# Kernel optimization log

Hardware: AMD Instinct MI355X
Metric: run time of the kernel (lower is better)

The kernel has to match this reference:

```python
import jax, jax.numpy as jnp
import numpy as np

S, V, H = 32, 16, 8            # hidden_scalars, hidden_vectors, num_heads
N, E = 10000, 100000           # nodes, edges
NRB, RH = 16, 64               # radial basis, radial MLP hidden
TH = S + 3 * V                 # packed irreps width (80)
WNUM = S * S + V * S + S * V + 2 * V * V  # TP weight_numel = 2560


def setup_inputs() -> dict:
    key = jax.random.key(0)
    ks = jax.random.split(key, 16)
    inp = {}
    inp["node_features"] = jax.random.normal(ks[0], (N, TH), jnp.float32)
    inp["edge_index"] = jax.random.randint(ks[1], (2, E), 0, N)
    inp["edge_sh"] = jax.random.normal(ks[2], (E, 4), jnp.float32)
    inp["edge_radial"] = jax.random.uniform(ks[3], (E, NRB), dtype=jnp.float32)
    inp["edge_envelope"] = jax.random.uniform(ks[4], (E,), dtype=jnp.float32)
    # radial MLP
    inp["W1"] = jax.random.normal(ks[5], (NRB, RH), jnp.float32) / np.sqrt(NRB)
    inp["b1"] = jnp.zeros((RH,), jnp.float32)
    inp["W2"] = jax.random.normal(ks[6], (RH, WNUM), jnp.float32) / np.sqrt(RH)
    inp["b2"] = jnp.zeros((WNUM,), jnp.float32)
    # attention query/key nets (scalar channels only)
    inp["Wq"] = jax.random.normal(ks[7], (S, H), jnp.float32) / np.sqrt(S)
    inp["bq"] = jnp.zeros((H,), jnp.float32)
    inp["Wk"] = jax.random.normal(ks[8], (S, H), jnp.float32) / np.sqrt(S)
    inp["bk"] = jnp.zeros((H,), jnp.float32)
    # equivariant linears (per-irrep channel mixing, e3nn style, no bias)
    inp["Wout_s"] = jax.random.normal(ks[9], (S, S), jnp.float32)
    inp["Wout_v"] = jax.random.normal(ks[10], (V, V), jnp.float32)
    inp["Wg_s"] = jax.random.normal(ks[11], (S, S + V), jnp.float32)
    inp["Wg_v"] = jax.random.normal(ks[12], (V, V), jnp.float32)
    # equivariant batch norm params
    inp["bn_ws"] = jnp.ones((S,), jnp.float32)
    inp["bn_bs"] = jnp.zeros((S,), jnp.float32)
    inp["bn_wv"] = jnp.ones((V,), jnp.float32)
    return inp


def _forward(node_features, edge_sh, edge_radial, edge_envelope,
             W1, b1, W2, b2, Wq, bq, Wk, bk,
             Wout_s, Wout_v, Wg_s, Wg_v, bn_ws, bn_bs, bn_wv, src, dst):
    # --- per-edge TP weights from radial MLP -> (E, WNUM), the big tensor ---
    tp_w = jax.nn.silu(edge_radial @ W1 + b1) @ W2 + b2
    offs = np.cumsum([0, S * S, V * S, S * V, V * V, V * V])
    WA = tp_w[:, offs[0]:offs[1]].reshape(-1, S, S)  # 0e x 0e -> 0e
    WB = tp_w[:, offs[1]:offs[2]].reshape(-1, V, S)  # 1o x 1o -> 0e
    WC = tp_w[:, offs[2]:offs[3]].reshape(-1, S, V)  # 0e x 1o -> 1o
    WD = tp_w[:, offs[3]:offs[4]].reshape(-1, V, V)  # 1o x 0e -> 1o
    WE = tp_w[:, offs[4]:offs[5]].reshape(-1, V, V)  # 1o x 1o -> 1o (cross)

    # --- gather source features, split irreps ---
    s_src = node_features[src, :S]                       # (E, S)
    v_src = node_features[src, S:].reshape(-1, V, 3)     # (E, V, 3)
    y0 = edge_sh[:, 0:1]                                 # (E, 1) l=0
    y1 = edge_sh[:, 1:4]                                 # (E, 3) l=1

    a0 = 1.0 / np.sqrt(S + V)       # path normalization, 0e output
    a1 = 1.0 / np.sqrt(S + 2 * V)   # path normalization, 1o output

    dot = (v_src * y1[:, None, :]).sum(-1) / np.sqrt(3.0)          # (E, V)
    msg_s = a0 * (jnp.einsum('es,esk->ek', s_src * y0, WA)
                  + jnp.einsum('ev,evk->ek', dot, WB))             # (E, S)
    crs = jnp.cross(v_src, y1[:, None, :]) / np.sqrt(2.0)          # (E, V, 3)
    msg_v = a1 * (jnp.einsum('es,ec,esk->ekc', s_src, y1, WC)
                  + jnp.einsum('evc,evk->ekc', v_src * y0[:, :, None], WD)
                  + jnp.einsum('evc,evk->ekc', crs, WE))           # (E, V, 3)
    messages = jnp.concatenate([msg_s, msg_v.reshape(-1, 3 * V)], axis=-1)

    # --- scatter-softmax attention over incoming edges per destination ---
    q = node_features[dst, :S] @ Wq + bq                 # (E, H)
    k = msg_s @ Wk + bk                                  # (E, H)
    logits = (q * k).sum(-1) / np.sqrt(H) + jnp.log(edge_envelope + 1e-8)
    mx = jax.ops.segment_max(logits, dst, num_segments=N)
    ex = jnp.exp(logits - mx[dst])
    den = jax.ops.segment_sum(ex, dst, num_segments=N)
    attn = ex / (den[dst] + 1e-8)                        # (E,)

    agg = jax.ops.segment_sum(attn[:, None] * messages, dst, num_segments=N)

    # --- equivariant output linear ---
    agg_s = agg[:, :S] @ Wout_s / np.sqrt(S)
    agg_v = jnp.einsum('nvc,vw->nwc', agg[:, S:].reshape(-1, V, 3), Wout_v) / np.sqrt(V)

    # --- gate ---
    gs = agg_s @ Wg_s / np.sqrt(S)                       # (N, S+V)
    gv = jnp.einsum('nvc,vw->nwc', agg_v, Wg_v) / np.sqrt(V)
    s = jax.nn.silu(gs[:, :S])
    g = jax.nn.sigmoid(gs[:, S:])
    v = g[:, :, None] * gv
    act = jnp.concatenate([s, v.reshape(-1, 3 * V)], axis=-1)

    # --- residual + equivariant batch norm ---
    x = act + node_features
    xs = x[:, :S]
    xv = x[:, S:].reshape(-1, V, 3)
    mean = xs.mean(0)
    var = xs.var(0)
    xs = (xs - mean) / jnp.sqrt(var + 1e-5) * bn_ws + bn_bs
    vn = (xv * xv).mean(-1).mean(0)                      # (V,) component norm
    xv = xv * (bn_wv / jnp.sqrt(vn + 1e-5))[None, :, None]
    return jnp.concatenate([xs, xv.reshape(-1, 3 * V)], axis=-1)


def reference(node_features, edge_index, edge_sh, edge_radial, edge_envelope,
              W1, b1, W2, b2, Wq, bq, Wk, bk,
              Wout_s, Wout_v, Wg_s, Wg_v, bn_ws, bn_bs, bn_wv):
    src, dst = edge_index[0], edge_index[1]
    return _forward(node_features, edge_sh, edge_radial, edge_envelope,
                    W1, b1, W2, b2, Wq, bq, Wk, bk,
                    Wout_s, Wout_v, Wg_s, Wg_v, bn_ws, bn_bs, bn_wv, src, dst)
```

## Files before the change

### kernel.cpp

```cpp
#include <hip/hip_runtime.h>
#include <math.h>

typedef __bf16 bf16x8 __attribute__((ext_vector_type(8)));
typedef __bf16 bf16x4 __attribute__((ext_vector_type(4)));
typedef float  f32x4  __attribute__((ext_vector_type(4)));
typedef float  f32x2  __attribute__((ext_vector_type(2)));
typedef unsigned long long u64x2 __attribute__((ext_vector_type(2)));

__device__ __forceinline__ float silu_f(float x){ return x / (1.f + __expf(-x)); }
__device__ __forceinline__ float sigm_f(float x){ return 1.f / (1.f + __expf(-x)); }

__device__ __forceinline__ float ntld_f(const float* p){
  return __builtin_nontemporal_load(p);
}
__device__ __forceinline__ float ntbf(const __bf16* p){
  unsigned short us = __builtin_nontemporal_load((const unsigned short*)p);
  union { unsigned u; float f; } cv; cv.u = ((unsigned)us) << 16;
  return cv.f;
}
__device__ __forceinline__ void nt_store_f(float* p, float v){
  __builtin_nontemporal_store(v, p);
}
__device__ __forceinline__ void nt_store_b8(__bf16* p, bf16x8 v){
  u64x2 u; __builtin_memcpy(&u, &v, 16);
  __builtin_nontemporal_store(u, (u64x2*)p);
}
__device__ __forceinline__ f32x2 b4lo(bf16x4 v){ f32x2 r; r[0]=(float)v[0]; r[1]=(float)v[1]; return r; }
__device__ __forceinline__ f32x2 b4hi(bf16x4 v){ f32x2 r; r[0]=(float)v[2]; r[1]=(float)v[3]; return r; }

__global__ void __launch_bounds__(256) k_setup(const float* __restrict__ W2,
    __bf16* __restrict__ W2t, const int* __restrict__ ei, int* __restrict__ cnt,
    const float* __restrict__ nf, const float* __restrict__ Wq,
    const float* __restrict__ bq, const float* __restrict__ Wk,
    const float* __restrict__ bk, float* __restrict__ kvt, float* __restrict__ carr,
    int nbPrep, int nbHist, int N, int E){
  int b = blockIdx.x, t = threadIdx.x;
  if (b < nbPrep){
    int gid = b*256 + t;
    int h = gid / 2560;
    int col = gid - h*2560;
    W2t[(size_t)(h>>5)*81920 + col*32 + (h&31)] = (__bf16)ntld_f(&W2[gid]);
    return;
  }
  if (b < nbPrep + nbHist){
    int e = (b - nbPrep)*256 + t;
    if (e < E) atomicAdd(&cnt[ei[E+e]], 1);
    return;
  }
  __shared__ float M[32][33];
  __shared__ float mb[32];
  __shared__ float nfl[64][33];
  __shared__ float bqbk_s;
  const int n0 = (b - nbPrep - nbHist)*64;
  for (int idx = t; idx < 1024; idx += 256){
    int s = idx >> 5, i = idx & 31;
    float acc = 0.f;
    #pragma unroll
    for (int j = 0; j < 8; ++j) acc += Wq[s*8+j]*Wk[i*8+j];
    M[s][i] = acc;
  }
  if (t < 32){
    float acc = 0.f;
    #pragma unroll
    for (int j = 0; j < 8; ++j) acc += Wq[t*8+j]*bk[j];
    mb[t] = acc;
  }
  if (t == 0){
    float acc = 0.f;
    #pragma unroll
    for (int j = 0; j < 8; ++j) acc += bq[j]*bk[j];
    bqbk_s = acc;
  }
  for (int idx = t; idx < 2048; idx += 256){
    int nl = idx >> 5, s = idx & 31;
    int n = n0 + nl;
    nfl[nl][s] = (n < N) ? nf[(size_t)n*80 + s] : 0.f;
  }
  __syncthreads();
  for (int idx = t; idx < 2048; idx += 256){
    int nl = idx >> 5, i = idx & 31;
    int n = n0 + nl;
    if (n < N){
      float acc = 0.f;
      #pragma unroll 8
      for (int s = 0; s < 32; ++s) acc += nfl[nl][s]*M[s][i];
      kvt[(size_t)n*32 + i] = acc;
    }
  }
  if (t < 64){
    int n = n0 + t;
    if (n < N){
      float acc = bqbk_s;
      #pragma unroll 8
      for (int s = 0; s < 32; ++s) acc += nfl[t][s]*mb[s];
      carr[n] = acc;
    }
  }
}

__global__ void __launch_bounds__(1024) k_scan(const int* __restrict__ cnt,
    int* __restrict__ cursor, float* __restrict__ bnacc, int N, int E){
  __shared__ int part[1024];
  int t = threadIdx.x;
  if (t < 80) bnacc[t] = 0.f;
  int chunk = (N + 1023) >> 10;
  int lo = t*chunk, hi = min(lo+chunk, N);
  int s = 0;
  for (int i = lo; i < hi; ++i) s += cnt[i];
  part[t] = s;
  __syncthreads();
  for (int off = 1; off < 1024; off <<= 1){
    int v = (t >= off) ? part[t-off] : 0;
    __syncthreads();
    part[t] += v;
    __syncthreads();
  }
  int base = (t == 0) ? 0 : part[t-1];
  for (int i = lo; i < hi; ++i){
    cursor[i] = base;
    base += cnt[i];
  }
}

__global__ void __launch_bounds__(256) k_prep(
    const float* __restrict__ nf, const int* __restrict__ ei,
    const float* __restrict__ sh, const float* __restrict__ radial,
    const float* __restrict__ W1, const float* __restrict__ b1,
    int* __restrict__ cursor,
    __bf16* __restrict__ uG, __bf16* __restrict__ cabG, __bf16* __restrict__ cvG,
    int* __restrict__ permG, int E, int NT)
{
  __shared__ float featT[80][65];
  __shared__ float radl[64][17];
  __shared__ float shlT[4][64];
  __shared__ float w1l[1024];
  __shared__ float b1l[64];
  __shared__ __align__(16) __bf16 u_l[64][72];
  __shared__ __align__(16) __bf16 cab_l[48][64];
  __shared__ __align__(16) __bf16 cv_l[64][3][64];
  __shared__ int src_l[64];

  const int t = threadIdx.x;
  const int e0 = blockIdx.x*64;
  const int tg0 = blockIdx.x*4;

  if (t < 64){
    int ee = e0 + t;
    if (ee < E){
      src_l[t] = ei[ee];
      permG[ee] = atomicAdd(&cursor[ei[(size_t)E+ee]], 1);
    } else src_l[t] = ei[E-1];
    b1l[t] = b1[t];
  }
  {
    int e = t >> 2, c = t & 3;
    int ec = min(e0+e, E-1);
    shlT[c][e] = ntld_f(&sh[(size_t)ec*4+c]);
  }
  for (int i = t; i < 1024; i += 256){
    int e = i >> 4, r = i & 15;
    int ec = min(e0+e, E-1);
    radl[e][r] = ntld_f(&radial[(size_t)ec*16+r]);
  }
  *(float4*)&w1l[t*4] = ((const float4*)W1)[t];
  __syncthreads();

  for (int i = t; i < 5120; i += 256){
    int e = i / 80, idx = i - e*80;
    featT[idx][e] = nf[(size_t)src_l[e]*80 + idx];
  }
  for (int i = t; i < 4096; i += 256){
    int e = i & 63, h = i >> 6;
    float acc = b1l[h];
    #pragma unroll
    for (int r = 0; r < 16; ++r) acc += radl[e][r]*w1l[r*64+h];
    u_l[e][h] = (__bf16)silu_f(acc);
  }
  __syncthreads();

  const float inv_s3 = 0.57735026918962576f;
  const float inv_s2 = 0.70710678118654752f;
  const float a0 = 0.14433756729740643f;
  const float a1 = 0.125f;

  for (int i = t; i < 3072; i += 256){
    int r = i >> 6, e = i & 63;
    float val;
    if (r < 32) val = a0 * shlT[0][e] * featT[r][e];
    else {
      int v = r - 32;
      float dot = (featT[32+v*3][e]*shlT[1][e] + featT[33+v*3][e]*shlT[2][e]
                 + featT[34+v*3][e]*shlT[3][e]) * inv_s3;
      val = a0 * dot;
    }
    cab_l[r][e] = (__bf16)val;
  }
  for (int i = t; i < 12288; i += 256){
    int e = i & 63, r = (i >> 6) & 63, c = i >> 12;
    float val;
    if (r < 32) val = a1 * shlT[1+c][e] * featT[r][e];
    else if (r < 48){
      int v = r - 32;
      val = a1 * shlT[0][e] * featT[32+v*3+c][e];
    } else {
      int v = r - 48;
      int c1 = c+1; if (c1 > 2) c1 -= 3;
      int c2 = c+2; if (c2 > 2) c2 -= 3;
      val = a1 * inv_s2 * (featT[32+v*3+c1][e]*shlT[1+c2][e]
                         - featT[32+v*3+c2][e]*shlT[1+c1][e]);
    }
    cv_l[r][c][e] = (__bf16)val;
  }
  __syncthreads();

  for (int i = t; i < 512; i += 256){
    int tl = i >> 7, rem = i & 127, k8 = rem >> 4, e = rem & 15;
    if (tg0 + tl < NT){
      bf16x8 v = *(const bf16x8*)&u_l[tl*16 + e][k8*8];
      *(bf16x8*)((char*)uG + (size_t)(tg0+tl)*2048 + k8*256 + e*16) = v;
    }
  }
  for (int i = t; i < 384; i += 256){
    int tl = i / 96, rem = i - tl*96, r = rem >> 1, h = rem & 1;
    if (tg0 + tl < NT){
      bf16x8 v = *(const bf16x8*)&cab_l[r][tl*16 + h*8];
      *(bf16x8*)((char*)cabG + (size_t)(tg0+tl)*1536 + r*32 + h*16) = v;
    }
  }
  for (int i = t; i < 1536; i += 256){
    int tl = i / 384, rem = i - tl*384, r = rem / 6, rem2 = rem - r*6,
        c = rem2 >> 1, h = rem2 & 1;
    if (tg0 + tl < NT){
      bf16x8 v = *(const bf16x8*)&cv_l[r][c][tl*16 + h*8];
      *(bf16x8*)((char*)cvG + (size_t)(tg0+tl)*6144 + r*96 + c*32 + h*16) = v;
    }
  }
}

#define LOAD_PANEL(BASE_IT, NITS) do {                                         \
    for (int idx = t; idx < (NITS)*128; idx += 1024){                          \
      int itl_ = idx >> 7, rem_ = idx & 127, half_ = rem_ >> 6, r6_ = rem_ & 63;\
      int col_ = r6_ >> 2, quad_ = r6_ & 3;                                    \
      *(float4*)(panel + itl_*2048 + half_*1024 + quad_*256 + col_*16) =       \
        *(const float4*)(w2b + half_*163840 + (size_t)((BASE_IT)+itl_)*1024    \
                         + col_*64 + quad_*16);                                \
    }                                                                          \
    for (int i = t; i < (NITS)*16; i += 1024) b2l[i] = b2[(BASE_IT)*16 + i];   \
  } while(0)

#define CAB_STAGE(TGC, BASE) do {                                              \
    bf16x8 x_ = *(const bf16x8*)(cabGb + (size_t)(TGC)*1536 + lane*16);        \
    bf16x4 y_ = *(const bf16x4*)(cabGb + (size_t)(TGC)*1536 + 1024 + lane*8);  \
    *(bf16x8*)(myCab + (BASE) + lane*16) = x_;                                 \
    *(bf16x4*)(myCab + (BASE) + 1024 + lane*8) = y_;                           \
  } while(0)

#define CV_STAGE_SUB(TGC, BASE, HALF, SUB) do {                                \
    const char* s_ = cvGb + (size_t)(TGC)*6144 + (HALF)*3072 + (SUB)*1536      \
                   + lane*24;                                                  \
    bf16x4 a_ = *(const bf16x4*)(s_);                                          \
    bf16x4 b_ = *(const bf16x4*)(s_ + 8);                                      \
    bf16x4 c_ = *(const bf16x4*)(s_ + 16);                                     \
    *(bf16x4*)(myCab + (BASE) + lane*24)      = a_;                            \
    *(bf16x4*)(myCab + (BASE) + lane*24 + 8)  = b_;                            \
    *(bf16x4*)(myCab + (BASE) + lane*24 + 16) = c_;                            \
  } while(0)

#define S_PAIR(SECOND, CBA, CBB, TA, TB) do {                                  \
    _Pragma("unroll 4")                                                        \
    for (int itl = 0; itl < 48; ++itl){                                        \
      bf16x8 B0_ = *(const bf16x8*)(panel + itl*2048 + laneOff);               \
      bf16x8 B1_ = *(const bf16x8*)(panel + itl*2048 + 1024 + laneOff);        \
      f32x4 dA_; dA_[0]=0;dA_[1]=0;dA_[2]=0;dA_[3]=0; f32x4 dB_ = dA_;         \
      dA_ = __builtin_amdgcn_mfma_f32_16x16x32_bf16(u##TA##_0, B0_, dA_, 0,0,0);\
      dB_ = __builtin_amdgcn_mfma_f32_16x16x32_bf16(u##TB##_0, B0_, dB_, 0,0,0);\
      dA_ = __builtin_amdgcn_mfma_f32_16x16x32_bf16(u##TA##_1, B1_, dA_, 0,0,0);\
      dB_ = __builtin_amdgcn_mfma_f32_16x16x32_bf16(u##TB##_1, B1_, dB_, 0,0,0);\
      const float bias_ = b2l[itl*16 + nlo];                                   \
      f32x2 bb_; bb_[0]=bias_; bb_[1]=bias_;                                   \
      f32x2 dAlo_ = __builtin_shufflevector(dA_,dA_,0,1) + bb_;                \
      f32x2 dAhi_ = __builtin_shufflevector(dA_,dA_,2,3) + bb_;                \
      f32x2 dBlo_ = __builtin_shufflevector(dB_,dB_,0,1) + bb_;                \
      f32x2 dBhi_ = __builtin_shufflevector(dB_,dB_,2,3) + bb_;                \
      const int r_ = (SECOND)*24 + (itl>>1);                                   \
      bf16x4 cA_ = *(const bf16x4*)(myCab + (CBA) + r_*32 + quad*8);           \
      bf16x4 cB_ = *(const bf16x4*)(myCab + (CBB) + r_*32 + quad*8);           \
      if (itl & 1){                                                            \
        s1l##TA += b4lo(cA_)*dAlo_; s1h##TA += b4hi(cA_)*dAhi_;                \
        s1l##TB += b4lo(cB_)*dBlo_; s1h##TB += b4hi(cB_)*dBhi_;                \
      } else {                                                                 \
        s0l##TA += b4lo(cA_)*dAlo_; s0h##TA += b4hi(cA_)*dAhi_;                \
        s0l##TB += b4lo(cB_)*dBlo_; s0h##TB += b4hi(cB_)*dBhi_;                \
      }                                                                        \
    }                                                                          \
  } while(0)

#define V_PAIR_SUB(SUB, TA, TB) do {                                           \
    _Pragma("unroll 4")                                                        \
    for (int il = 0; il < 16; ++il){                                           \
      const int gitl = (SUB)*16 + il;                                          \
      bf16x8 B0_ = *(const bf16x8*)(panel + gitl*2048 + laneOff);              \
      bf16x8 B1_ = *(const bf16x8*)(panel + gitl*2048 + 1024 + laneOff);       \
      f32x4 dA_; dA_[0]=0;dA_[1]=0;dA_[2]=0;dA_[3]=0; f32x4 dB_ = dA_;         \
      dA_ = __builtin_amdgcn_mfma_f32_16x16x32_bf16(u##TA##_0, B0_, dA_, 0,0,0);\
      dB_ = __builtin_amdgcn_mfma_f32_16x16x32_bf16(u##TB##_0, B0_, dB_, 0,0,0);\
      dA_ = __builtin_amdgcn_mfma_f32_16x16x32_bf16(u##TA##_1, B1_, dA_, 0,0,0);\
      dB_ = __builtin_amdgcn_mfma_f32_16x16x32_bf16(u##TB##_1, B1_, dB_, 0,0,0);\
      const float bias_ = b2l[gitl*16 + nlo];                                  \
      f32x2 bb_; bb_[0]=bias_; bb_[1]=bias_;                                   \
      f32x2 dAlo_ = __builtin_shufflevector(dA_,dA_,0,1) + bb_;                \
      f32x2 dAhi_ = __builtin_shufflevector(dA_,dA_,2,3) + bb_;                \
      f32x2 dBlo_ = __builtin_shufflevector(dB_,dB_,0,1) + bb_;                \
      f32x2 dBhi_ = __builtin_shufflevector(dB_,dB_,2,3) + bb_;                \
      const char* cbA_ = myCab + il*96;                                        \
      const char* cbB_ = myCab + 1536 + il*96;                                 \
      bf16x4 q0_ = *(const bf16x4*)(cbA_ + quad*8);                            \
      bf16x4 q1_ = *(const bf16x4*)(cbA_ + 32 + quad*8);                       \
      bf16x4 q2_ = *(const bf16x4*)(cbA_ + 64 + quad*8);                       \
      v0l##TA += b4lo(q0_)*dAlo_; v0h##TA += b4hi(q0_)*dAhi_;                  \
      v1l##TA += b4lo(q1_)*dAlo_; v1h##TA += b4hi(q1_)*dAhi_;                  \
      v2l##TA += b4lo(q2_)*dAlo_; v2h##TA += b4hi(q2_)*dAhi_;                  \
      q0_ = *(const bf16x4*)(cbB_ + quad*8);                                   \
      q1_ = *(const bf16x4*)(cbB_ + 32 + quad*8);                              \
      q2_ = *(const bf16x4*)(cbB_ + 64 + quad*8);                              \
      v0l##TB += b4lo(q0_)*dBlo_; v0h##TB += b4hi(q0_)*dBhi_;                  \
      v1l##TB += b4lo(q1_)*dBlo_; v1h##TB += b4hi(q1_)*dBhi_;                  \
      v2l##TB += b4lo(q2_)*dBlo_; v2h##TB += b4hi(q2_)*dBhi_;                  \
    }                                                                          \
  } while(0)

#define S_FLUSH(TG, S0LO, S0HI, S1LO, S1HI) do {                               \
      myOut[(eb+0)*56 + nlo] = S0LO[0];                                        \
      myOut[(eb+1)*56 + nlo] = S0LO[1];                                        \
      myOut[(eb+2)*56 + nlo] = S0HI[0];                                        \
      myOut[(eb+3)*56 + nlo] = S0HI[1];                                        \
      myOut[(eb+0)*56 + 16+nlo] = S1LO[0];                                     \
      myOut[(eb+1)*56 + 16+nlo] = S1LO[1];                                     \
      myOut[(eb+2)*56 + 16+nlo] = S1HI[0];                                     \
      myOut[(eb+3)*56 + 16+nlo] = S1HI[1];                                     \
      const int e0e = (TG)*16;                                                 \
      { int e = lane>>2, seg = lane&3, eg = e0e + e;                           \
        if (eg < E){                                                           \
          f32x4 m0 = *(const f32x4*)&myOut[e*56 + seg*8];                      \
          f32x4 m1 = *(const f32x4*)&myOut[e*56 + seg*8 + 4];                  \
          bf16x8 o; o[0]=(__bf16)m0[0]; o[1]=(__bf16)m0[1];                    \
          o[2]=(__bf16)m0[2]; o[3]=(__bf16)m0[3]; o[4]=(__bf16)m1[0];          \
          o[5]=(__bf16)m1[1]; o[6]=(__bf16)m1[2]; o[7]=(__bf16)m1[3];          \
          nt_store_b8(msgs + (size_t)permG[eg]*80 + seg*8, o);                 \
        } }                                                                    \
      for (int r8 = 0; r8 < 2; ++r8){                                          \
        int e = r8*8 + (lane>>3), kq = lane&7, eg = e0e + e;                   \
        f32x4 ms = *(const f32x4*)&myOut[e*56 + kq*4];                         \
        int dn = ei[(size_t)E + min(eg, E-1)];                                 \
        const float* kvp = kvt + (size_t)dn*32 + kq*4;                         \
        float part = ms[0]*kvp[0]+ms[1]*kvp[1]+ms[2]*kvp[2]+ms[3]*kvp[3];      \
        part += __shfl_xor(part, 1);                                           \
        part += __shfl_xor(part, 2);                                           \
        part += __shfl_xor(part, 4);                                           \
        if (kq == 0 && eg < E){                                                \
          float lg = (part + carr[dn]) * 0.35355339059327373f                  \
                   + logf(ntld_f(&env[eg]) + 1e-8f);                           \
          nt_store_f(&logits_s[permG[eg]], lg);                                \
        } }                                                                    \
  } while(0)

#define V_FLUSH(TG, V0LO, V0HI, V1LO, V1HI, V2LO, V2HI) do {                   \
      const int cb2 = nlo*3;                                                   \
      myOut[(eb+0)*56 + cb2+0] = V0LO[0];                                      \
      myOut[(eb+1)*56 + cb2+0] = V0LO[1];                                      \
      myOut[(eb+2)*56 + cb2+0] = V0HI[0];                                      \
      myOut[(eb+3)*56 + cb2+0] = V0HI[1];                                      \
      myOut[(eb+0)*56 + cb2+1] = V1LO[0];                                      \
      myOut[(eb+1)*56 + cb2+1] = V1LO[1];                                      \
      myOut[(eb+2)*56 + cb2+1] = V1HI[0];                                      \
      myOut[(eb+3)*56 + cb2+1] = V1HI[1];                                      \
      myOut[(eb+0)*56 + cb2+2] = V2LO[0];                                      \
      myOut[(eb+1)*56 + cb2+2] = V2LO[1];                                      \
      myOut[(eb+2)*56 + cb2+2] = V2HI[0];                                      \
      myOut[(eb+3)*56 + cb2+2] = V2HI[1];                                      \
      const int e0e = (TG)*16;                                                 \
      for (int i = lane; i < 96; i += 64){                                     \
        int e = i/6, seg = i - (i/6)*6, eg = e0e + e;                          \
        if (eg < E){                                                           \
          f32x4 m0 = *(const f32x4*)&myOut[e*56 + seg*8];                      \
          f32x4 m1 = *(const f32x4*)&myOut[e*56 + seg*8 + 4];                  \
          bf16x8 o; o[0]=(__bf16)m0[0]; o[1]=(__bf16)m0[1];                    \
          o[2]=(__bf16)m0[2]; o[3]=(__bf16)m0[3]; o[4]=(__bf16)m1[0];          \
          o[5]=(__bf16)m1[1]; o[6]=(__bf16)m1[2]; o[7]=(__bf16)m1[3];          \
          nt_store_b8(msgs + (size_t)permG[eg]*80 + 32 + seg*8, o);            \
        } }                                                                    \
  } while(0)

__global__ void __launch_bounds__(1024, 4) k_edge(
    const __bf16* __restrict__ W2t, const float* __restrict__ b2,
    const __bf16* __restrict__ uG, const __bf16* __restrict__ cabG,
    const __bf16* __restrict__ cvG, const int* __restrict__ ei,
    const int* __restrict__ permG, const float* __restrict__ kvt,
    const float* __restrict__ carr, const float* __restrict__ env,
    __bf16* __restrict__ msgs, float* __restrict__ logits_s, int E, int NT)
{
  __shared__ __align__(16) char panel[98304];
  __shared__ __align__(16) char wstage[16][3584];
  __shared__ float b2l[768];

  const int t = threadIdx.x;
  const int lane = t & 63;
  const int wv   = t >> 6;
  const int quad = lane >> 4;
  const int nlo  = lane & 15;
  const int wgid = blockIdx.x*16 + wv;
  const int laneOff = quad*256 + nlo*16;
  const int uOff    = quad*256 + nlo*16;
  char*  myCab = wstage[wv];
  float* myOut = (float*)wstage[wv];
  const char* w2b   = (const char*)W2t;
  const char* uGb   = (const char*)uG;
  const char* cabGb = (const char*)cabG;
  const char* cvGb  = (const char*)cvG;

  const int tA = wgid, tB = wgid + 4096;
  const bool hA = tA < NT, hB = tB < NT;
  const int cA = min(tA, NT-1), cB = min(tB, NT-1);

  const bf16x8 uA_0 = *(const bf16x8*)(uGb + (size_t)cA*2048 + uOff);
  const bf16x8 uA_1 = *(const bf16x8*)(uGb + (size_t)cA*2048 + 1024 + uOff);
  const bf16x8 uB_0 = *(const bf16x8*)(uGb + (size_t)cB*2048 + uOff);
  const bf16x8 uB_1 = *(const bf16x8*)(uGb + (size_t)cB*2048 + 1024 + uOff);

  f32x2 s0lA={0,0}, s0hA={0,0}, s1lA={0,0}, s1hA={0,0};
  f32x2 s0lB={0,0}, s0hB={0,0}, s1lB={0,0}, s1hB={0,0};

  const int eb = quad*4;

  LOAD_PANEL(0, 48);
  CAB_STAGE(cA, 0); CAB_STAGE(cB, 1536);
  __syncthreads();
  S_PAIR(0, 0, 1536, A, B);
  __syncthreads();
  LOAD_PANEL(48, 48);
  __syncthreads();
  S_PAIR(1, 0, 1536, A, B);
  if (hA) S_FLUSH(tA, s0lA, s0hA, s1lA, s1hA);
  if (hB) S_FLUSH(tB, s0lB, s0hB, s1lB, s1hB);
  __syncthreads();

  f32x2 v0lA={0,0}, v0hA={0,0}, v1lA={0,0}, v1hA={0,0}, v2lA={0,0}, v2hA={0,0};
  f32x2 v0lB={0,0}, v0hB={0,0}, v1lB={0,0}, v1hB={0,0}, v2lB={0,0}, v2hB={0,0};

  LOAD_PANEL(96, 32);
  __syncthreads();
  CV_STAGE_SUB(cA, 0, 0, 0); CV_STAGE_SUB(cB, 1536, 0, 0);
  V_PAIR_SUB(0, A, B);
  CV_STAGE_SUB(cA, 0, 0, 1); CV_STAGE_SUB(cB, 1536, 0, 1);
  V_PAIR_SUB(1, A, B);
  __syncthreads();
  LOAD_PANEL(128, 32);
  __syncthreads();
  CV_STAGE_SUB(cA, 0, 1, 0); CV_STAGE_SUB(cB, 1536, 1, 0);
  V_PAIR_SUB(0, A, B);
  CV_STAGE_SUB(cA, 0, 1, 1); CV_STAGE_SUB(cB, 1536, 1, 1);
  V_PAIR_SUB(1, A, B);
  if (hA) V_FLUSH(tA, v0lA, v0hA, v1lA, v1hA, v2lA, v2hA);
  if (hB) V_FLUSH(tB, v0lB, v0hB, v1lB, v1hB, v2lB, v2hB);
}

__global__ void __launch_bounds__(256) k_agg(
    const __bf16* __restrict__ msgs, const float* __restrict__ logits_s,
    const int* __restrict__ cursor, const float* __restrict__ nf,
    const float* __restrict__ Wout_s, const float* __restrict__ Wout_v,
    const float* __restrict__ Wg_s, const float* __restrict__ Wg_v,
    float* __restrict__ xbuf, float* __restrict__ bnacc, int N)
{
  __shared__ float aggl[4][80];
  __shared__ float t1[4][96];
  __shared__ float t2[4][96];
  __shared__ float bnl[80];
  const int t = threadIdx.x, l = t & 63, wv = t >> 6;
  const int n = blockIdx.x*4 + wv;
  const bool act = (n < N);
  const int nc = act ? n : (N-1);
  if (t < 80) bnl[t] = 0.f;

  const int r0 = (nc == 0) ? 0 : cursor[nc-1];
  const int r1 = cursor[nc];
  const int deg = act ? (r1 - r0) : 0;

  float mym = -3.4e38f;
  for (int i = l; i < deg; i += 64) mym = fmaxf(mym, logits_s[r0+i]);
  #pragma unroll
  for (int s = 32; s; s >>= 1) mym = fmaxf(mym, __shfl_xor(mym, s));
  float denp = 0.f, acc0 = 0.f, acc1 = 0.f;
  for (int c0 = 0; c0 < deg; c0 += 64){
    const int len = min(64, deg - c0);
    float ex = 0.f;
    if (l < len) ex = __expf(logits_s[r0+c0+l] - mym);
    denp += ex;
    for (int j0 = 0; j0 < len; j0 += 4){
      const int jn = len - j0;
      const __bf16* base = msgs + (size_t)(r0+c0+j0)*80;
      float v0=0,v1=0,v2=0,v3=0, w0=0,w1=0,w2=0,w3=0;
      float a0_=0,a1_=0,a2_=0,a3_=0;
      v0 = ntbf(&base[l]); if (l < 16) w0 = ntbf(&base[64+l]); a0_ = __shfl(ex, j0);
      if (jn > 1){ v1 = ntbf(&base[80+l]);  if (l < 16) w1 = ntbf(&base[144+l]); a1_ = __shfl(ex, j0+1); }
      if (jn > 2){ v2 = ntbf(&base[160+l]); if (l < 16) w2 = ntbf(&base[224+l]); a2_ = __shfl(ex, j0+2); }
      if (jn > 3){ v3 = ntbf(&base[240+l]); if (l < 16) w3 = ntbf(&base[304+l]); a3_ = __shfl(ex, j0+3); }
      acc0 += a0_*v0 + a1_*v1 + a2_*v2 + a3_*v3;
      if (l < 16) acc1 += a0_*w0 + a1_*w1 + a2_*w2 + a3_*w3;
    }
  }
  #pragma unroll
  for (int s = 32; s; s >>= 1) denp += __shfl_xor(denp, s);
  const float inv = 1.f/(denp + 1e-8f);
  aggl[wv][l] = acc0 * inv;
  if (l < 16) aggl[wv][64+l] = acc1 * inv;
  __syncthreads();

  const float* arow = &aggl[wv][0];
  const float iS = 0.17677669529663687f;
  const float iV = 0.25f;
  for (int o = l; o < 80; o += 64){
    float val = 0.f;
    if (o < 32){
      for (int s = 0; s < 32; ++s) val += arow[s]*Wout_s[s*32+o];
      val *= iS;
    } else {
      int w = (o-32)/3, c = (o-32)-w*3;
      for (int v = 0; v < 16; ++v) val += arow[32+v*3+c]*Wout_v[v*16+w];
      val *= iV;
    }
    t1[wv][o] = val;
  }
  __syncthreads();
  for (int o = l; o < 96; o += 64){
    float val = 0.f;
    if (o < 48){
      for (int k = 0; k < 32; ++k) val += t1[wv][k]*Wg_s[k*48+o];
      val *= iS;
    } else {
      int w = (o-48)/3, c = (o-48)-w*3;
      for (int v = 0; v < 16; ++v) val += t1[wv][32+v*3+c]*Wg_v[v*16+w];
      val *= iV;
    }
    t2[wv][o] = val;
  }
  __syncthreads();
  for (int o = l; o < 80; o += 64){
    float x;
    if (o < 32){
      x = silu_f(t2[wv][o]) + nf[(size_t)nc*80+o];
      if (act){
        nt_store_f(&xbuf[(size_t)n*80+o], x);
        atomicAdd(&bnl[o], x);
        atomicAdd(&bnl[32+o], x*x);
      }
    } else {
      int w = (o-32)/3;
      x = sigm_f(t2[wv][32+w]) * t2[wv][48+(o-32)] + nf[(size_t)nc*80+o];
      if (act){
        nt_store_f(&xbuf[(size_t)n*80+o], x);
        atomicAdd(&bnl[64+w], x*x);
      }
    }
  }
  __syncthreads();
  if (t < 80) atomicAdd(&bnacc[t], bnl[t]);
}

__global__ void __launch_bounds__(256) k_out(const float* __restrict__ xbuf,
    const float* __restrict__ bnacc,
    const float* __restrict__ bn_ws, const float* __restrict__ bn_bs,
    const float* __restrict__ bn_wv, float* __restrict__ out, int N){
  __shared__ float coef[80];
  int t = threadIdx.x;
  float fN = (float)N;
  if (t < 32){
    float mean = bnacc[t]/fN;
    float var = bnacc[32+t]/fN - mean*mean;
    float cm = bn_ws[t]*rsqrtf(var + 1e-5f);
    coef[t] = cm;
    coef[32+t] = bn_bs[t] - mean*cm;
  } else if (t < 48){
    int v = t - 32;
    coef[64+v] = bn_wv[v]*rsqrtf(bnacc[64+v]/(3.f*fN) + 1e-5f);
  }
  __syncthreads();
  int i = blockIdx.x*256 + t;
  if (i >= N*80) return;
  int o = i - (i/80)*80;
  float x = ntld_f(&xbuf[i]);
  nt_store_f(&out[i], (o < 32) ? (x*coef[o] + coef[32+o]) : (x*coef[64+(o-32)/3]));
}

extern "C" void kernel_launch(void* const* d_in, const int* in_sizes, int n_in,
                              void* d_out, int out_size, void* d_ws, size_t ws_size,
                              hipStream_t stream) {
  const float* nf     = (const float*)d_in[0];
  const int*   ei     = (const int*)  d_in[1];
  const float* sh     = (const float*)d_in[2];
  const float* radial = (const float*)d_in[3];
  const float* env    = (const float*)d_in[4];
  const float* W1     = (const float*)d_in[5];
  const float* b1     = (const float*)d_in[6];
  const float* W2     = (const float*)d_in[7];
  const float* b2     = (const float*)d_in[8];
  const float* Wq     = (const float*)d_in[9];
  const float* bq     = (const float*)d_in[10];
  const float* Wk     = (const float*)d_in[11];
  const float* bk     = (const float*)d_in[12];
  const float* Wout_s = (const float*)d_in[13];
  const float* Wout_v = (const float*)d_in[14];
  const float* Wg_s   = (const float*)d_in[15];
  const float* Wg_v   = (const float*)d_in[16];
  const float* bn_ws  = (const float*)d_in[17];
  const float* bn_bs  = (const float*)d_in[18];
  const float* bn_wv  = (const float*)d_in[19];

  const int E = in_sizes[4];
  const int N = in_sizes[0] / 80;
  const int NT = (E + 15)/16;

  float* ws = (float*)d_ws;
  size_t off = 0;
  __bf16* w2t    = (__bf16*)(ws + off); off += 81920;
  __bf16* msgs   = (__bf16*)(ws + off); off += (size_t)E*40;
  float* logits_s= ws + off; off += E;
  int* cnt       = (int*)(ws + off); off += N;
  int* cursor    = (int*)(ws + off); off += N;
  float* xbuf    = ws + off; off += (size_t)N*80;
  float* bnacc   = ws + off; off += 80;
  float* kvt     = ws + off; off += (size_t)N*32;
  float* carr    = ws + off; off += N;
  int* permG     = (int*)(ws + off); off += E;
  __bf16* uG     = (__bf16*)(ws + off); off += (size_t)NT*512;
  __bf16* cabG   = (__bf16*)(ws + off); off += (size_t)NT*384;
  __bf16* cvG    = (__bf16*)(ws + off); off += (size_t)NT*1536;

  hipMemsetAsync(cnt, 0, (size_t)N*sizeof(int), stream);

  const int nbPrep = 640;
  const int nbHist = (E + 255)/256;
  const int nbKv   = (N + 63)/64;
  k_setup<<<nbPrep + nbHist + nbKv, 256, 0, stream>>>(W2, w2t, ei, cnt,
      nf, Wq, bq, Wk, bk, kvt, carr, nbPrep, nbHist, N, E);
  k_scan<<<1, 1024, 0, stream>>>(cnt, cursor, bnacc, N, E);
  k_prep<<<(E + 63)/64, 256, 0, stream>>>(nf, ei, sh, radial, W1, b1, cursor,
      uG, cabG, cvG, permG, E, NT);
  k_edge<<<256, 1024, 0, stream>>>(w2t, b2, uG, cabG, cvG, ei, permG,
      kvt, carr, env, msgs, logits_s, E, NT);
  k_agg<<<(N + 3)/4, 256, 0, stream>>>(msgs, logits_s, cursor, nf,
      Wout_s, Wout_v, Wg_s, Wg_v, xbuf, bnacc, N);
  k_out<<<(N*80 + 255)/256, 256, 0, stream>>>(xbuf, bnacc, bn_ws, bn_bs, bn_wv,
      (float*)d_out, N);
}
```

Measured before the change: 355.5 us.

## Precompute b2 bias contributions per edge in prep, interleave A/B coefficient staging

The constant b2 bias term of the per-edge TP weights is split out algebraically. Its contraction with the per-edge coefficients is computed once in k_prep and stored as per-tile bias arrays, which the edge kernel adds at flush time. This removes the per-iteration bias loads and adds from the MFMA inner loops. The coefficient staging in shared memory is also re-laid out so tiles A and B sit interleaved, letting one 16-byte LDS read serve both tiles. The cost is extra global traffic for the bias arrays (about 5 KB per 16-edge tile) and extra scalar work in k_prep.

```diff
diff --git a/kernel.cpp b/kernel.cpp
--- a/kernel.cpp
+++ b/kernel.cpp
@@ -126,8 +126,9 @@
     const float* __restrict__ nf, const int* __restrict__ ei,
     const float* __restrict__ sh, const float* __restrict__ radial,
     const float* __restrict__ W1, const float* __restrict__ b1,
-    int* __restrict__ cursor,
+    const float* __restrict__ b2, int* __restrict__ cursor,
     __bf16* __restrict__ uG, __bf16* __restrict__ cabG, __bf16* __restrict__ cvG,
+    float* __restrict__ biasSG, float* __restrict__ biasVG,
     int* __restrict__ permG, int E, int NT)
 {
   __shared__ float featT[80][65];
@@ -235,6 +236,31 @@
       *(bf16x8*)((char*)cvG + (size_t)(tg0+tl)*6144 + r*96 + c*32 + h*16) = v;
     }
   }
+  float* b2s = &featT[0][0];
+  for (int i = t; i < 2560; i += 256) b2s[i] = b2[i];
+  __syncthreads();
+  for (int i = t; i < 2048; i += 256){
+    int e = i >> 5, k = i & 31;
+    int hi = k >> 4, kk = k & 15;
+    float acc = 0.f;
+    #pragma unroll 8
+    for (int r = 0; r < 48; ++r)
+      acc += (float)cab_l[r][e] * b2s[(2*r+hi)*16 + kk];
+    int tl = e >> 4, et = e & 15;
+    if (tg0 + tl < NT)
+      biasSG[(size_t)(tg0+tl)*512 + et*32 + k] = acc;
+  }
+  for (int i = t; i < 3072; i += 256){
+    int e = i / 48, col = i - (i/48)*48;
+    int w = col/3, c = col - w*3;
+    float acc = 0.f;
+    #pragma unroll 8
+    for (int r = 0; r < 64; ++r)
+      acc += (float)cv_l[r][c][e] * b2s[(96+r)*16 + w];
+    int tl = e >> 4, et = e & 15;
+    if (tg0 + tl < NT)
+      biasVG[(size_t)(tg0+tl)*768 + et*48 + col] = acc;
+  }
 }
 
 #define LOAD_PANEL(BASE_IT, NITS) do {                                         \
@@ -245,28 +271,33 @@
         *(const float4*)(w2b + half_*163840 + (size_t)((BASE_IT)+itl_)*1024    \
                          + col_*64 + quad_*16);                                \
     }                                                                          \
-    for (int i = t; i < (NITS)*16; i += 1024) b2l[i] = b2[(BASE_IT)*16 + i];   \
   } while(0)
 
-#define CAB_STAGE(TGC, BASE) do {                                              \
-    bf16x8 x_ = *(const bf16x8*)(cabGb + (size_t)(TGC)*1536 + lane*16);        \
-    bf16x4 y_ = *(const bf16x4*)(cabGb + (size_t)(TGC)*1536 + 1024 + lane*8);  \
-    *(bf16x8*)(myCab + (BASE) + lane*16) = x_;                                 \
-    *(bf16x4*)(myCab + (BASE) + 1024 + lane*8) = y_;                           \
+#define CAB_STAGE2() do {                                                      \
+    for (int i = lane; i < 384; i += 64){                                      \
+      int tb_ = i & 1; int c_ = i >> 1;                                        \
+      int r_ = c_ >> 2, q_ = c_ & 3;                                           \
+      const char* s_ = cabGb + (size_t)(tb_ ? cB : cA)*1536 + r_*32 + q_*8;    \
+      unsigned long long v_ = *(const unsigned long long*)s_;                  \
+      *(unsigned long long*)(myCab + r_*64 + q_*16 + tb_*8) = v_;              \
+    }                                                                          \
   } while(0)
 
-#define CV_STAGE_SUB(TGC, BASE, HALF, SUB) do {                                \
-    const char* s_ = cvGb + (size_t)(TGC)*6144 + (HALF)*3072 + (SUB)*1536      \
-                   + lane*24;                                                  \
-    bf16x4 a_ = *(const bf16x4*)(s_);                                          \
-    bf16x4 b_ = *(const bf16x4*)(s_ + 8);                                      \
-    bf16x4 c_ = *(const bf16x4*)(s_ + 16);                                     \
-    *(bf16x4*)(myCab + (BASE) + lane*24)      = a_;                            \
-    *(bf16x4*)(myCab + (BASE) + lane*24 + 8)  = b_;                            \
-    *(bf16x4*)(myCab + (BASE) + lane*24 + 16) = c_;                            \
+#define CV_STAGE2(SUB, HALF) do {                                              \
+    for (int i = lane; i < 384; i += 64){                                      \
+      int tb_ = i & 1; int x_ = i >> 1;                                        \
+      int c3_ = x_ % 3; int rem_ = x_ / 3;                                     \
+      int il_ = rem_ >> 2, q_ = rem_ & 3;                                      \
+      const char* s_ = cvGb + (size_t)(tb_ ? cB : cA)*6144 + (HALF)*3072       \
+                     + ((SUB)*16 + il_)*96 + c3_*32 + q_*8;                    \
+      unsigned long long v_ = *(const unsigned long long*)s_;                  \
+      char* d_ = (c3_ < 2) ? (myCab + tb_*1024 + il_*64 + q_*16 + c3_*8)       \
+                           : (myCab + 2048 + il_*64 + q_*16 + tb_*8);          \
+      *(unsigned long long*)d_ = v_;                                           \
+    }                                                                          \
   } while(0)
 
-#define S_PAIR(SECOND, CBA, CBB, TA, TB) do {                                  \
+#define S_PAIR(SECOND, TA, TB) do {                                            \
     _Pragma("unroll 4")                                                        \
     for (int itl = 0; itl < 48; ++itl){                                        \
       bf16x8 B0_ = *(const bf16x8*)(panel + itl*2048 + laneOff);               \
@@ -276,15 +307,14 @@
       dB_ = __builtin_amdgcn_mfma_f32_16x16x32_bf16(u##TB##_0, B0_, dB_, 0,0,0);\
       dA_ = __builtin_amdgcn_mfma_f32_16x16x32_bf16(u##TA##_1, B1_, dA_, 0,0,0);\
       dB_ = __builtin_amdgcn_mfma_f32_16x16x32_bf16(u##TB##_1, B1_, dB_, 0,0,0);\
-      const float bias_ = b2l[itl*16 + nlo];                                   \
-      f32x2 bb_; bb_[0]=bias_; bb_[1]=bias_;                                   \
-      f32x2 dAlo_ = __builtin_shufflevector(dA_,dA_,0,1) + bb_;                \
-      f32x2 dAhi_ = __builtin_shufflevector(dA_,dA_,2,3) + bb_;                \
-      f32x2 dBlo_ = __builtin_shufflevector(dB_,dB_,0,1) + bb_;                \
-      f32x2 dBhi_ = __builtin_shufflevector(dB_,dB_,2,3) + bb_;                \
+      f32x2 dAlo_ = __builtin_shufflevector(dA_,dA_,0,1);                      \
+      f32x2 dAhi_ = __builtin_shufflevector(dA_,dA_,2,3);                      \
+      f32x2 dBlo_ = __builtin_shufflevector(dB_,dB_,0,1);                      \
+      f32x2 dBhi_ = __builtin_shufflevector(dB_,dB_,2,3);                      \
       const int r_ = (SECOND)*24 + (itl>>1);                                   \
-      bf16x4 cA_ = *(const bf16x4*)(myCab + (CBA) + r_*32 + quad*8);           \
-      bf16x4 cB_ = *(const bf16x4*)(myCab + (CBB) + r_*32 + quad*8);           \
+      bf16x8 c8_ = *(const bf16x8*)(myCab + r_*64 + quad*16);                  \
+      bf16x4 cA_ = __builtin_shufflevector(c8_, c8_, 0,1,2,3);                 \
+      bf16x4 cB_ = __builtin_shufflevector(c8_, c8_, 4,5,6,7);                 \
       if (itl & 1){                                                            \
         s1l##TA += b4lo(cA_)*dAlo_; s1h##TA += b4hi(cA_)*dAhi_;                \
         s1l##TB += b4lo(cB_)*dBlo_; s1h##TB += b4hi(cB_)*dBhi_;                \
@@ -306,26 +336,25 @@
       dB_ = __builtin_amdgcn_mfma_f32_16x16x32_bf16(u##TB##_0, B0_, dB_, 0,0,0);\
       dA_ = __builtin_amdgcn_mfma_f32_16x16x32_bf16(u##TA##_1, B1_, dA_, 0,0,0);\
       dB_ = __builtin_amdgcn_mfma_f32_16x16x32_bf16(u##TB##_1, B1_, dB_, 0,0,0);\
-      const float bias_ = b2l[gitl*16 + nlo];                                  \
-      f32x2 bb_; bb_[0]=bias_; bb_[1]=bias_;                                   \
-      f32x2 dAlo_ = __builtin_shufflevector(dA_,dA_,0,1) + bb_;                \
-      f32x2 dAhi_ = __builtin_shufflevector(dA_,dA_,2,3) + bb_;                \
-      f32x2 dBlo_ = __builtin_shufflevector(dB_,dB_,0,1) + bb_;                \
-      f32x2 dBhi_ = __builtin_shufflevector(dB_,dB_,2,3) + bb_;                \
-      const char* cbA_ = myCab + il*96;                                        \
-      const char* cbB_ = myCab + 1536 + il*96;                                 \
-      bf16x4 q0_ = *(const bf16x4*)(cbA_ + quad*8);                            \
-      bf16x4 q1_ = *(const bf16x4*)(cbA_ + 32 + quad*8);                       \
-      bf16x4 q2_ = *(const bf16x4*)(cbA_ + 64 + quad*8);                       \
-      v0l##TA += b4lo(q0_)*dAlo_; v0h##TA += b4hi(q0_)*dAhi_;                  \
-      v1l##TA += b4lo(q1_)*dAlo_; v1h##TA += b4hi(q1_)*dAhi_;                  \
-      v2l##TA += b4lo(q2_)*dAlo_; v2h##TA += b4hi(q2_)*dAhi_;                  \
-      q0_ = *(const bf16x4*)(cbB_ + quad*8);                                   \
-      q1_ = *(const bf16x4*)(cbB_ + 32 + quad*8);                              \
-      q2_ = *(const bf16x4*)(cbB_ + 64 + quad*8);                              \
-      v0l##TB += b4lo(q0_)*dBlo_; v0h##TB += b4hi(q0_)*dBhi_;                  \
-      v1l##TB += b4lo(q1_)*dBlo_; v1h##TB += b4hi(q1_)*dBhi_;                  \
-      v2l##TB += b4lo(q2_)*dBlo_; v2h##TB += b4hi(q2_)*dBhi_;                  \
+      f32x2 dAlo_ = __builtin_shufflevector(dA_,dA_,0,1);                      \
+      f32x2 dAhi_ = __builtin_shufflevector(dA_,dA_,2,3);                      \
+      f32x2 dBlo_ = __builtin_shufflevector(dB_,dB_,0,1);                      \
+      f32x2 dBhi_ = __builtin_shufflevector(dB_,dB_,2,3);                      \
+      bf16x8 cA01_ = *(const bf16x8*)(myCab + il*64 + quad*16);                \
+      bf16x8 cB01_ = *(const bf16x8*)(myCab + 1024 + il*64 + quad*16);         \
+      bf16x8 c2_   = *(const bf16x8*)(myCab + 2048 + il*64 + quad*16);         \
+      bf16x4 q0A_ = __builtin_shufflevector(cA01_, cA01_, 0,1,2,3);            \
+      bf16x4 q1A_ = __builtin_shufflevector(cA01_, cA01_, 4,5,6,7);            \
+      bf16x4 q0B_ = __builtin_shufflevector(cB01_, cB01_, 0,1,2,3);            \
+      bf16x4 q1B_ = __builtin_shufflevector(cB01_, cB01_, 4,5,6,7);            \
+      bf16x4 q2A_ = __builtin_shufflevector(c2_, c2_, 0,1,2,3);                \
+      bf16x4 q2B_ = __builtin_shufflevector(c2_, c2_, 4,5,6,7);                \
+      v0l##TA += b4lo(q0A_)*dAlo_; v0h##TA += b4hi(q0A_)*dAhi_;                \
+      v1l##TA += b4lo(q1A_)*dAlo_; v1h##TA += b4hi(q1A_)*dAhi_;                \
+      v2l##TA += b4lo(q2A_)*dAlo_; v2h##TA += b4hi(q2A_)*dAhi_;                \
+      v0l##TB += b4lo(q0B_)*dBlo_; v0h##TB += b4hi(q0B_)*dBhi_;                \
+      v1l##TB += b4lo(q1B_)*dBlo_; v1h##TB += b4hi(q1B_)*dBhi_;                \
+      v2l##TB += b4lo(q2B_)*dBlo_; v2h##TB += b4hi(q2B_)*dBhi_;                \
     }                                                                          \
   } while(0)
 
@@ -341,8 +370,9 @@
       const int e0e = (TG)*16;                                                 \
       { int e = lane>>2, seg = lane&3, eg = e0e + e;                           \
         if (eg < E){                                                           \
-          f32x4 m0 = *(const f32x4*)&myOut[e*56 + seg*8];                      \
-          f32x4 m1 = *(const f32x4*)&myOut[e*56 + seg*8 + 4];                  \
+          const float* bS_ = biasSG + (size_t)(TG)*512 + lane*8;               \
+          f32x4 m0 = *(const f32x4*)&myOut[e*56 + seg*8]     + *(const f32x4*)bS_;\
+          f32x4 m1 = *(const f32x4*)&myOut[e*56 + seg*8 + 4] + *(const f32x4*)(bS_+4);\
           bf16x8 o; o[0]=(__bf16)m0[0]; o[1]=(__bf16)m0[1];                    \
           o[2]=(__bf16)m0[2]; o[3]=(__bf16)m0[3]; o[4]=(__bf16)m1[0];          \
           o[5]=(__bf16)m1[1]; o[6]=(__bf16)m1[2]; o[7]=(__bf16)m1[3];          \
@@ -351,6 +381,7 @@
       for (int r8 = 0; r8 < 2; ++r8){                                          \
         int e = r8*8 + (lane>>3), kq = lane&7, eg = e0e + e;                   \
         f32x4 ms = *(const f32x4*)&myOut[e*56 + kq*4];                         \
+        ms += *(const f32x4*)(biasSG + (size_t)(TG)*512 + r8*256 + lane*4);    \
         int dn = ei[(size_t)E + min(eg, E-1)];                                 \
         const float* kvp = kvt + (size_t)dn*32 + kq*4;                         \
         float part = ms[0]*kvp[0]+ms[1]*kvp[1]+ms[2]*kvp[2]+ms[3]*kvp[3];      \
@@ -382,8 +413,9 @@
       for (int i = lane; i < 96; i += 64){                                     \
         int e = i/6, seg = i - (i/6)*6, eg = e0e + e;                          \
         if (eg < E){                                                           \
-          f32x4 m0 = *(const f32x4*)&myOut[e*56 + seg*8];                      \
-          f32x4 m1 = *(const f32x4*)&myOut[e*56 + seg*8 + 4];                  \
+          const float* bV_ = biasVG + (size_t)(TG)*768 + i*8;                  \
+          f32x4 m0 = *(const f32x4*)&myOut[e*56 + seg*8]     + *(const f32x4*)bV_;\
+          f32x4 m1 = *(const f32x4*)&myOut[e*56 + seg*8 + 4] + *(const f32x4*)(bV_+4);\
           bf16x8 o; o[0]=(__bf16)m0[0]; o[1]=(__bf16)m0[1];                    \
           o[2]=(__bf16)m0[2]; o[3]=(__bf16)m0[3]; o[4]=(__bf16)m1[0];          \
           o[5]=(__bf16)m1[1]; o[6]=(__bf16)m1[2]; o[7]=(__bf16)m1[3];          \
@@ -392,16 +424,17 @@
   } while(0)
 
 __global__ void __launch_bounds__(1024, 4) k_edge(
-    const __bf16* __restrict__ W2t, const float* __restrict__ b2,
+    const __bf16* __restrict__ W2t,
     const __bf16* __restrict__ uG, const __bf16* __restrict__ cabG,
-    const __bf16* __restrict__ cvG, const int* __restrict__ ei,
+    const __bf16* __restrict__ cvG,
+    const float* __restrict__ biasSG, const float* __restrict__ biasVG,
+    const int* __restrict__ ei,
     const int* __restrict__ permG, const float* __restrict__ kvt,
     const float* __restrict__ carr, const float* __restrict__ env,
     __bf16* __restrict__ msgs, float* __restrict__ logits_s, int E, int NT)
 {
   __shared__ __align__(16) char panel[98304];
   __shared__ __align__(16) char wstage[16][3584];
-  __shared__ float b2l[768];
 
   const int t = threadIdx.x;
   const int lane = t & 63;
@@ -433,13 +466,13 @@
   const int eb = quad*4;
 
   LOAD_PANEL(0, 48);
-  CAB_STAGE(cA, 0); CAB_STAGE(cB, 1536);
-  __syncthreads();
-  S_PAIR(0, 0, 1536, A, B);
+  CAB_STAGE2();
+  __syncthreads();
+  S_PAIR(0, A, B);
   __syncthreads();
   LOAD_PANEL(48, 48);
   __syncthreads();
-  S_PAIR(1, 0, 1536, A, B);
+  S_PAIR(1, A, B);
   if (hA) S_FLUSH(tA, s0lA, s0hA, s1lA, s1hA);
   if (hB) S_FLUSH(tB, s0lB, s0hB, s1lB, s1hB);
   __syncthreads();
@@ -449,16 +482,16 @@
 
   LOAD_PANEL(96, 32);
   __syncthreads();
-  CV_STAGE_SUB(cA, 0, 0, 0); CV_STAGE_SUB(cB, 1536, 0, 0);
+  CV_STAGE2(0, 0);
   V_PAIR_SUB(0, A, B);
-  CV_STAGE_SUB(cA, 0, 0, 1); CV_STAGE_SUB(cB, 1536, 0, 1);
+  CV_STAGE2(1, 0);
   V_PAIR_SUB(1, A, B);
   __syncthreads();
   LOAD_PANEL(128, 32);
   __syncthreads();
-  CV_STAGE_SUB(cA, 0, 1, 0); CV_STAGE_SUB(cB, 1536, 1, 0);
+  CV_STAGE2(0, 1);
   V_PAIR_SUB(0, A, B);
-  CV_STAGE_SUB(cA, 0, 1, 1); CV_STAGE_SUB(cB, 1536, 1, 1);
+  CV_STAGE2(1, 1);
   V_PAIR_SUB(1, A, B);
   if (hA) V_FLUSH(tA, v0lA, v0hA, v1lA, v1hA, v2lA, v2hA);
   if (hB) V_FLUSH(tB, v0lB, v0hB, v1lB, v1hB, v2lB, v2hB);
@@ -634,6 +667,8 @@
   __bf16* uG     = (__bf16*)(ws + off); off += (size_t)NT*512;
   __bf16* cabG   = (__bf16*)(ws + off); off += (size_t)NT*384;
   __bf16* cvG    = (__bf16*)(ws + off); off += (size_t)NT*1536;
+  float* biasSG  = ws + off; off += (size_t)NT*512;
+  float* biasVG  = ws + off; off += (size_t)NT*768;
 
   hipMemsetAsync(cnt, 0, (size_t)N*sizeof(int), stream);
 
@@ -643,10 +678,10 @@
   k_setup<<<nbPrep + nbHist + nbKv, 256, 0, stream>>>(W2, w2t, ei, cnt,
       nf, Wq, bq, Wk, bk, kvt, carr, nbPrep, nbHist, N, E);
   k_scan<<<1, 1024, 0, stream>>>(cnt, cursor, bnacc, N, E);
-  k_prep<<<(E + 63)/64, 256, 0, stream>>>(nf, ei, sh, radial, W1, b1, cursor,
-      uG, cabG, cvG, permG, E, NT);
-  k_edge<<<256, 1024, 0, stream>>>(w2t, b2, uG, cabG, cvG, ei, permG,
-      kvt, carr, env, msgs, logits_s, E, NT);
+  k_prep<<<(E + 63)/64, 256, 0, stream>>>(nf, ei, sh, radial, W1, b1, b2,
+      cursor, uG, cabG, cvG, biasSG, biasVG, permG, E, NT);
+  k_edge<<<256, 1024, 0, stream>>>(w2t, uG, cabG, cvG, biasSG, biasVG,
+      ei, permG, kvt, carr, env, msgs, logits_s, E, NT);
   k_agg<<<(N + 3)/4, 256, 0, stream>>>(msgs, logits_s, cursor, nf,
       Wout_s, Wout_v, Wg_s, Wg_v, xbuf, bnacc, N);
   k_out<<<(N*80 + 255)/256, 256, 0, stream>>>(xbuf, bnacc, bn_ws, bn_bs, bn_wv,
```

New measurement: 438.1 us. +23.2%, slower.
